# Optimization experiments

Hardware: AMD Instinct MI355X
Metric: run time of the kernel (lower is better)

The kernel has to match this reference:

```python
import jax, jax.numpy as jnp
import numpy as np

N_NODES = 50000
N_EDGES = 1600000
D_IN = 64
D_OUT = 64
N_REL = 32


def setup_inputs() -> dict:
    key = jax.random.key(0)
    k_h, k_w, k_src, k_dst, k_rel, k_norm = jax.random.split(key, 6)
    h = jax.random.normal(k_h, (N_NODES, D_IN), dtype=jnp.float32)
    W = jax.random.normal(k_w, (N_REL, D_IN, D_OUT), dtype=jnp.float32) * 0.05
    src = jax.random.randint(k_src, (N_EDGES,), 0, N_NODES, dtype=jnp.int32)
    dst = jax.random.randint(k_dst, (N_EDGES,), 0, N_NODES, dtype=jnp.int32)
    rel_type = jax.random.randint(k_rel, (N_EDGES,), 0, N_REL, dtype=jnp.int32)
    norm = jax.random.uniform(k_norm, (N_EDGES,), dtype=jnp.float32)
    return {"h": h, "W": W, "src": src, "dst": dst, "rel_type": rel_type, "norm": norm}


def reference(h, W, src, dst, rel_type, norm):
    # R-GCN message passing (is_input=False branch):
    #   msg_e = (W[rel_type_e] applied to h[src_e]) * norm_e
    #   h'_v  = sum_{e: dst_e = v} msg_e
    # Instead of gathering a [E, D_IN, D_OUT] weight tensor per edge (26 GB),
    # precompute h @ W for all (node, relation) pairs -- mathematically
    # identical since W[r] h[n] = (hW)[n, r] -- then gather per edge.
    n_nodes = h.shape[0]
    per_node_rel = jnp.einsum('ni,rio->nro', h, W)            # [N, R, D_OUT]
    msg = per_node_rel[src, rel_type] * norm[:, None]         # [E, D_OUT]
    out = jax.ops.segment_sum(msg, dst, num_segments=n_nodes)  # [N, D_OUT]
    return out
```

## Files before the change

### kernel.cpp

```cpp
#include <hip/hip_runtime.h>


#define N_NODES 50000
#define N_EDGES 1600000
#define D 64
#define N_REL 32

#define BSHIFT 7
#define NPB 128
#define NB 391
#define EPB 4096
#define SC_BLOCKS 391
#define SORT_CAP 6144
#define NKEY 256

typedef __attribute__((ext_vector_type(8))) __bf16 bf16x8;
typedef __attribute__((ext_vector_type(4))) __bf16 bf16x4;
typedef __attribute__((ext_vector_type(4))) float f32x4;
typedef __attribute__((ext_vector_type(4))) _Float16 f16x4;

static __device__ inline unsigned short f16_bits(_Float16 v) {
    union { _Float16 f; unsigned short u; } cv; cv.f = v; return cv.u;
}
static __device__ inline _Float16 bits_f16(unsigned short u) {
    union { _Float16 f; unsigned short u; } cv; cv.u = u; return cv.f;
}


__global__ __launch_bounds__(512) void k_zeroc(int* __restrict__ gcnt) {
    if (threadIdx.x < NB) gcnt[threadIdx.x] = 0;
}

__global__ __launch_bounds__(256) void k_hist2(const int* __restrict__ dst,
                                               int* __restrict__ gcnt) {
    __shared__ int lc[NB];
    for (int b = threadIdx.x; b < NB; b += 256) lc[b] = 0;
    __syncthreads();
    const int e0 = blockIdx.x * EPB;
    #pragma unroll
    for (int j = 0; j < 16; ++j) {
        int e = e0 + j * 256 + threadIdx.x;
        if (e < N_EDGES) atomicAdd(&lc[dst[e] >> BSHIFT], 1);
    }
    __syncthreads();
    for (int b = threadIdx.x; b < NB; b += 256)
        if (lc[b]) atomicAdd(&gcnt[b], lc[b]);
}

__global__ __launch_bounds__(512) void k_scanc(const int* __restrict__ gcnt,
                                               int* __restrict__ base,
                                               int* __restrict__ cur) {
    const int t = threadIdx.x;
    const int lane = t & 63;
    const int w = t >> 6;
    int v = (t < NB) ? gcnt[t] : 0;
    int x = v;
    #pragma unroll
    for (int d = 1; d < 64; d <<= 1) {
        int n = __shfl_up(x, d, 64);
        if (lane >= d) x += n;
    }
    __shared__ int wt[8];
    if (lane == 63) wt[w] = x;
    __syncthreads();
    if (t == 0) {
        int run = 0;
        #pragma unroll
        for (int i = 0; i < 8; ++i) { int tmp = wt[i]; wt[i] = run; run += tmp; }
    }
    __syncthreads();
    int excl = x - v + wt[w];
    if (t < NB) { base[t] = excl; cur[t] = excl; }
    if (t == NB - 1) base[NB] = excl + v;
}

__global__ __launch_bounds__(256) void k_scatter2(
        const int* __restrict__ src, const int* __restrict__ dst,
        const int* __restrict__ rel, const float* __restrict__ norm,
        int* __restrict__ cur, int2* __restrict__ pay) {
    __shared__ int cnt[NB];
    __shared__ int bl[NB + 1];
    __shared__ int gb[NB];
    __shared__ unsigned short bid[EPB];
    __shared__ int2 stage[EPB];
    __shared__ int wt[8];

    const int t = threadIdx.x;
    const int lane = t & 63;
    const int w = t >> 6;
    const int e0 = blockIdx.x * EPB;

    for (int b = t; b < NB; b += 256) cnt[b] = 0;
    __syncthreads();

    #pragma unroll
    for (int j = 0; j < 16; ++j) {
        int e = e0 + j * 256 + t;
        if (e < N_EDGES) atomicAdd(&cnt[dst[e] >> BSHIFT], 1);
    }
    __syncthreads();

    {
        int x0 = (t < NB) ? cnt[t] : 0;
        int x1 = (t + 256 < NB) ? cnt[t + 256] : 0;
        int s0 = x0, s1 = x1;
        #pragma unroll
        for (int d = 1; d < 64; d <<= 1) {
            int n0 = __shfl_up(s0, d, 64);
            int n1 = __shfl_up(s1, d, 64);
            if (lane >= d) { s0 += n0; s1 += n1; }
        }
        if (lane == 63) { wt[w] = s0; wt[4 + w] = s1; }
        __syncthreads();
        if (t == 0) {
            int run = 0;
            #pragma unroll
            for (int i = 0; i < 8; ++i) { int tmp = wt[i]; wt[i] = run; run += tmp; }
        }
        __syncthreads();
        int ex0 = s0 - x0 + wt[w];
        int ex1 = s1 - x1 + wt[4 + w];
        if (t < NB) bl[t] = ex0;
        if (t + 256 < NB) bl[t + 256] = ex1;
        if (t == 0) {
            int tot = (e0 + EPB <= N_EDGES) ? EPB : (N_EDGES > e0 ? N_EDGES - e0 : 0);
            bl[NB] = tot;
        }
    }
    __syncthreads();

    for (int b = t; b < NB; b += 256) {
        int c = bl[b + 1] - bl[b];
        gb[b] = c ? atomicAdd(&cur[b], c) : 0;
    }
    for (int b = t; b < NB; b += 256) cnt[b] = 0;
    __syncthreads();

    #pragma unroll
    for (int j = 0; j < 16; ++j) {
        int e = e0 + j * 256 + t;
        if (e < N_EDGES) {
            int dv = dst[e];
            int b = dv >> BSHIFT;
            int r = atomicAdd(&cnt[b], 1);
            int pos = bl[b] + r;
            stage[pos] = make_int2(((dv & (NPB - 1)) << 21) | (rel[e] << 16) | src[e],
                                   __float_as_int(norm[e]));
            bid[pos] = (unsigned short)b;
        }
    }
    __syncthreads();

    const int total = bl[NB];
    for (int p = t; p < total; p += 256) {
        int b = bid[p];
        pay[gb[b] + (p - bl[b])] = stage[p];
    }
}

__global__ __launch_bounds__(512) void k_sort(
        const int* __restrict__ base, int2* __restrict__ pay,
        int* __restrict__ runs) {
    __shared__ int2 stage[SORT_CAP];
    __shared__ int cnt[8][NKEY];
    __shared__ int wb[8][NKEY];
    __shared__ int kbase[NKEY];
    __shared__ int wsum[8];

    const int t = threadIdx.x;
    const int lane = t & 63;
    const int w = t >> 6;
    const int b = blockIdx.x;
    const int s = base[b];
    const int e = base[b + 1];
    const int n = min(e - s, SORT_CAP);

    for (int j = t; j < 8 * NKEY; j += 512) ((int*)cnt)[j] = 0;
    __syncthreads();

    for (int j = t; j < n; j += 512) {
        int2 p = pay[s + j];
        stage[j] = p;
        int key = (((p.x >> 25) & 7) << 5) | ((p.x >> 16) & 31);
        atomicAdd(&cnt[w][key], 1);
    }
    __syncthreads();

    int tot = 0;
    if (t < NKEY) {
        #pragma unroll
        for (int ww = 0; ww < 8; ++ww) tot += cnt[ww][t];
    }
    int x = tot;
    #pragma unroll
    for (int d = 1; d < 64; d <<= 1) {
        int nn = __shfl_up(x, d, 64);
        if (lane >= d) x += nn;
    }
    if (lane == 63) wsum[w] = x;
    __syncthreads();
    if (t == 0) {
        int run = 0;
        #pragma unroll
        for (int i = 0; i < 8; ++i) { int tmp = wsum[i]; wsum[i] = run; run += tmp; }
    }
    __syncthreads();
    int excl = x - tot + wsum[w];
    if (t < NKEY) kbase[t] = excl;
    __syncthreads();

    if (t < NKEY) {
        int run = kbase[t];
        #pragma unroll
        for (int ww = 0; ww < 8; ++ww) { wb[ww][t] = run; run += cnt[ww][t]; }
        runs[b * (NKEY + 1) + t] = s + kbase[t];
    }
    if (t == 0) runs[b * (NKEY + 1) + NKEY] = s + n;
    __syncthreads();
    for (int j = t; j < 8 * NKEY; j += 512) ((int*)cnt)[j] = 0;
    __syncthreads();

    for (int j = t; j < n; j += 512) {
        int2 p = stage[j];
        int key = (((p.x >> 25) & 7) << 5) | ((p.x >> 16) & 31);
        int pos = wb[w][key] + atomicAdd(&cnt[w][key], 1);
        pay[s + pos] = p;
    }
}

__global__ __launch_bounds__(256) void k_wconv(const float* __restrict__ W,
                                               __bf16* __restrict__ Wfrag) {
    const int r = blockIdx.x;
    const int lane = threadIdx.x & 63;
    const int jj = (threadIdx.x >> 6) * 2;
    const int q = lane >> 4;
    const int m = lane & 15;
    const float* Wr = W + (size_t)r * D * D;
    #pragma unroll
    for (int kt = 0; kt < 2; ++kt) {
        #pragma unroll
        for (int ot = 0; ot < 4; ++ot) {
            size_t dbase = ((((size_t)r * 2 + kt) * 4 + ot) * 64 + lane) * 8 + jj;
            Wfrag[dbase]     = (__bf16)Wr[(kt * 32 + q * 8 + jj) * D + ot * 16 + m];
            Wfrag[dbase + 1] = (__bf16)Wr[(kt * 32 + q * 8 + jj + 1) * D + ot * 16 + m];
        }
    }
}

__global__ __launch_bounds__(512) void k_hconv(const float* __restrict__ h,
                                               __bf16* __restrict__ hbf) {
    int idx = blockIdx.x * 512 + threadIdx.x;
    if (idx < N_NODES * 16) {
        float4 v = ((const float4*)h)[idx];
        bf16x4 o;
        o[0] = (__bf16)v.x; o[1] = (__bf16)v.y; o[2] = (__bf16)v.z; o[3] = (__bf16)v.w;
        ((bf16x4*)hbf)[idx] = o;
    }
}

__global__ __launch_bounds__(512) void k_fuse(
        const unsigned short* __restrict__ hbf, const __bf16* __restrict__ Wfrag,
        const int* __restrict__ runs, const int2* __restrict__ pay,
        float* __restrict__ out) {
    __shared__ int runsL[NKEY + 1];
    __shared__ __align__(16) unsigned short wbuf[2][4096];

    const int t = threadIdx.x;
    const int lane = t & 63;
    const int w = t >> 6;
    const int m = lane & 15;
    const int q = lane >> 4;
    const int b = blockIdx.x;

    for (int j = t; j < NKEY + 1; j += 512) runsL[j] = runs[b * (NKEY + 1) + j];
    ((bf16x8*)wbuf[0])[t] = ((const bf16x8*)Wfrag)[t];
    __syncthreads();

    const f32x4 vzero = {0.f, 0.f, 0.f, 0.f};
    f32x4 acc2[4];
    #pragma unroll
    for (int ot = 0; ot < 4; ++ot) acc2[ot] = vzero;

    const int kb = w * 32;

    int pr = 0, ptl = 0, prs = 0, pre_ = 0;
    while (pr < N_REL) { prs = runsL[kb + pr]; pre_ = runsL[kb + pr + 1]; if (pre_ > prs) break; ++pr; }

    int cr = N_REL, cmask = 0;
    int2 p_cur; bf16x8 a0c, a1c;
    int nrel = N_REL, nmask = 0;
    int2 p_nxt;

    if (pr < N_REL) {
        int ei = prs + ptl * 16 + m;
        p_cur = pay[min(ei, pre_ - 1)];
        cmask = (ei < pre_);
        cr = pr;
        ++ptl;
        if (prs + ptl * 16 >= pre_) {
            ++pr; ptl = 0;
            while (pr < N_REL) { prs = runsL[kb + pr]; pre_ = runsL[kb + pr + 1]; if (pre_ > prs) break; ++pr; }
        }
        const unsigned short* hrow = hbf + ((size_t)(p_cur.x & 0xFFFF) << 6);
        a0c = *(const bf16x8*)(hrow + q * 8);
        a1c = *(const bf16x8*)(hrow + 32 + q * 8);
        if (pr < N_REL) {
            int ei2 = prs + ptl * 16 + m;
            p_nxt = pay[min(ei2, pre_ - 1)];
            nmask = (ei2 < pre_);
            nrel = pr;
            ++ptl;
            if (prs + ptl * 16 >= pre_) {
                ++pr; ptl = 0;
                while (pr < N_REL) { prs = runsL[kb + pr]; pre_ = runsL[kb + pr + 1]; if (pre_ > prs) break; ++pr; }
            }
        }
    }

    for (int r = 0; r < N_REL; ++r) {
        bf16x8 stg;
        if (r + 1 < N_REL) stg = ((const bf16x8*)Wfrag)[(r + 1) * 512 + t];

        if (cr == r) {
            const unsigned short* wbp = wbuf[r & 1];
            bf16x8 wf[2][4];
            #pragma unroll
            for (int kt = 0; kt < 2; ++kt)
                #pragma unroll
                for (int ot = 0; ot < 4; ++ot)
                    wf[kt][ot] = *(const bf16x8*)(wbp + ((kt * 4 + ot) * 64 + lane) * 8);

            while (cr == r) {
                int2 p_b = p_nxt;
                int brel = nrel, bmask = nmask;
                bf16x8 a0n, a1n;
                if (brel < N_REL) {
                    const unsigned short* hrn = hbf + ((size_t)(p_b.x & 0xFFFF) << 6);
                    a0n = *(const bf16x8*)(hrn + q * 8);
                    a1n = *(const bf16x8*)(hrn + 32 + q * 8);
                }
                if (pr < N_REL) {
                    int ei2 = prs + ptl * 16 + m;
                    p_nxt = pay[min(ei2, pre_ - 1)];
                    nmask = (ei2 < pre_);
                    nrel = pr;
                    ++ptl;
                    if (prs + ptl * 16 >= pre_) {
                        ++pr; ptl = 0;
                        while (pr < N_REL) { prs = runsL[kb + pr]; pre_ = runsL[kb + pr + 1]; if (pre_ > prs) break; ++pr; }
                    }
                } else {
                    nrel = N_REL;
                }

                float nvf = cmask ? __int_as_float(p_cur.y) : 0.f;
                int meta = (((p_cur.x >> 21) & 15) << 16) | f16_bits((_Float16)nvf);

                f32x4 c1[4];
                #pragma unroll
                for (int ot = 0; ot < 4; ++ot) {
                    c1[ot] = __builtin_amdgcn_mfma_f32_16x16x32_bf16(a0c, wf[0][ot], vzero, 0, 0, 0);
                    c1[ot] = __builtin_amdgcn_mfma_f32_16x16x32_bf16(a1c, wf[1][ot], c1[ot], 0, 0, 0);
                }

                f16x4 a2;
                #pragma unroll
                for (int j = 0; j < 4; ++j) {
                    int sm = __shfl(meta, q * 4 + j, 64);
                    _Float16 nv = bits_f16((unsigned short)(sm & 0xFFFF));
                    a2[j] = ((sm >> 16) == m) ? nv : (_Float16)0.f;
                }

                #pragma unroll
                for (int ot = 0; ot < 4; ++ot) {
                    f16x4 b2;
                    b2[0] = (_Float16)c1[ot][0];
                    b2[1] = (_Float16)c1[ot][1];
                    b2[2] = (_Float16)c1[ot][2];
                    b2[3] = (_Float16)c1[ot][3];
                    acc2[ot] = __builtin_amdgcn_mfma_f32_16x16x16f16(a2, b2, acc2[ot], 0, 0, 0);
                }

                p_cur = p_b; cmask = bmask; cr = brel;
                a0c = a0n; a1c = a1n;
            }
        }

        if (r + 1 < N_REL) ((bf16x8*)wbuf[(r + 1) & 1])[t] = stg;
        __syncthreads();
    }

    const int node_base = b * NPB + w * 16;
    #pragma unroll
    for (int reg = 0; reg < 4; ++reg) {
        int node = node_base + q * 4 + reg;
        if (node < N_NODES) {
            float* orow = out + (size_t)node * D + m;
            #pragma unroll
            for (int ot = 0; ot < 4; ++ot)
                orow[ot * 16] = acc2[ot][reg];
        }
    }
}

extern "C" void kernel_launch(void* const* d_in, const int* in_sizes, int n_in,
                              void* d_out, int out_size, void* d_ws, size_t ws_size,
                              hipStream_t stream) {
    const float* h    = (const float*)d_in[0];
    const float* W    = (const float*)d_in[1];
    const int*   src  = (const int*)d_in[2];
    const int*   dst  = (const int*)d_in[3];
    const int*   rel  = (const int*)d_in[4];
    const float* norm = (const float*)d_in[5];
    float* out = (float*)d_out;

    char* ws = (char*)d_ws;
    int*    gcnt  = (int*)(ws);
    int*    base  = (int*)(ws + 0x1000);
    int*    cur   = (int*)(ws + 0x2000);
    int*    runs  = (int*)(ws + 0x3000);
    int2*   pay   = (int2*)(ws + 0x100000);
    __bf16* Wfrag = (__bf16*)(ws + 0xD40000);
    __bf16* hbf   = (__bf16*)(ws + 0xD80000);

    k_zeroc<<<1, 512, 0, stream>>>(gcnt);
    k_wconv<<<N_REL, 256, 0, stream>>>(W, Wfrag);
    k_hconv<<<1563, 512, 0, stream>>>(h, hbf);
    k_hist2<<<SC_BLOCKS, 256, 0, stream>>>(dst, gcnt);
    k_scanc<<<1, 512, 0, stream>>>(gcnt, base, cur);
    k_scatter2<<<SC_BLOCKS, 256, 0, stream>>>(src, dst, rel, norm, cur, pay);
    k_sort<<<NB, 512, 0, stream>>>(base, pay, runs);
    k_fuse<<<NB, 512, 0, stream>>>((const unsigned short*)hbf, Wfrag, runs, pay, out);
}
```

Before: 215.8 us.

## Replace histogram+scan with fixed-capacity buckets and fuse init kernels

Removes the destination histogram, scan and zeroing kernels by giving each bucket a fixed slot of capacity BCAP and initializing cursors to b*BCAP. Merges the h and W bf16 conversions and cursor init into a single launch. This cuts a full pass over dst, a serial scan kernel and several launch gaps, but assumes no bucket exceeds 6144 edges, and a skewed graph would overflow silently.

```diff
diff --git a/kernel.cpp b/kernel.cpp
--- a/kernel.cpp
+++ b/kernel.cpp
@@ -11,8 +11,12 @@
 #define NB 391
 #define EPB 4096
 #define SC_BLOCKS 391
+#define BCAP 6144
 #define SORT_CAP 6144
 #define NKEY 256
+
+#define HCONV_BLOCKS 1563
+#define INIT_BLOCKS (HCONV_BLOCKS + N_REL + 1)
 
 typedef __attribute__((ext_vector_type(8))) __bf16 bf16x8;
 typedef __attribute__((ext_vector_type(4))) __bf16 bf16x4;
@@ -27,51 +31,37 @@
 }
 
 
-__global__ __launch_bounds__(512) void k_zeroc(int* __restrict__ gcnt) {
-    if (threadIdx.x < NB) gcnt[threadIdx.x] = 0;
-}
-
-__global__ __launch_bounds__(256) void k_hist2(const int* __restrict__ dst,
-                                               int* __restrict__ gcnt) {
-    __shared__ int lc[NB];
-    for (int b = threadIdx.x; b < NB; b += 256) lc[b] = 0;
-    __syncthreads();
-    const int e0 = blockIdx.x * EPB;
-    #pragma unroll
-    for (int j = 0; j < 16; ++j) {
-        int e = e0 + j * 256 + threadIdx.x;
-        if (e < N_EDGES) atomicAdd(&lc[dst[e] >> BSHIFT], 1);
-    }
-    __syncthreads();
-    for (int b = threadIdx.x; b < NB; b += 256)
-        if (lc[b]) atomicAdd(&gcnt[b], lc[b]);
-}
-
-__global__ __launch_bounds__(512) void k_scanc(const int* __restrict__ gcnt,
-                                               int* __restrict__ base,
-                                               int* __restrict__ cur) {
-    const int t = threadIdx.x;
-    const int lane = t & 63;
-    const int w = t >> 6;
-    int v = (t < NB) ? gcnt[t] : 0;
-    int x = v;
-    #pragma unroll
-    for (int d = 1; d < 64; d <<= 1) {
-        int n = __shfl_up(x, d, 64);
-        if (lane >= d) x += n;
-    }
-    __shared__ int wt[8];
-    if (lane == 63) wt[w] = x;
-    __syncthreads();
-    if (t == 0) {
-        int run = 0;
-        #pragma unroll
-        for (int i = 0; i < 8; ++i) { int tmp = wt[i]; wt[i] = run; run += tmp; }
-    }
-    __syncthreads();
-    int excl = x - v + wt[w];
-    if (t < NB) { base[t] = excl; cur[t] = excl; }
-    if (t == NB - 1) base[NB] = excl + v;
+__global__ __launch_bounds__(512) void k_init(
+        const float* __restrict__ h, __bf16* __restrict__ hbf,
+        const float* __restrict__ W, __bf16* __restrict__ Wfrag,
+        int* __restrict__ cur) {
+    const int blk = blockIdx.x;
+    if (blk < HCONV_BLOCKS) {
+        int idx = blk * 512 + threadIdx.x;
+        if (idx < N_NODES * 16) {
+            float4 v = ((const float4*)h)[idx];
+            bf16x4 o;
+            o[0] = (__bf16)v.x; o[1] = (__bf16)v.y; o[2] = (__bf16)v.z; o[3] = (__bf16)v.w;
+            ((bf16x4*)hbf)[idx] = o;
+        }
+    } else if (blk < HCONV_BLOCKS + N_REL) {
+        const int r = blk - HCONV_BLOCKS;
+        const int lane = threadIdx.x & 63;
+        const int jj = threadIdx.x >> 6;
+        const int q = lane >> 4;
+        const int m = lane & 15;
+        const float* Wr = W + (size_t)r * D * D;
+        #pragma unroll
+        for (int kt = 0; kt < 2; ++kt) {
+            #pragma unroll
+            for (int ot = 0; ot < 4; ++ot) {
+                size_t dbase = ((((size_t)r * 2 + kt) * 4 + ot) * 64 + lane) * 8 + jj;
+                Wfrag[dbase] = (__bf16)Wr[(kt * 32 + q * 8 + jj) * D + ot * 16 + m];
+            }
+        }
+    } else {
+        if (threadIdx.x < NB) cur[threadIdx.x] = threadIdx.x * BCAP;
+    }
 }
 
 __global__ __launch_bounds__(256) void k_scatter2(
@@ -159,7 +149,7 @@
 }
 
 __global__ __launch_bounds__(512) void k_sort(
-        const int* __restrict__ base, int2* __restrict__ pay,
+        const int* __restrict__ cur, int2* __restrict__ pay,
         int* __restrict__ runs) {
     __shared__ int2 stage[SORT_CAP];
     __shared__ int cnt[8][NKEY];
@@ -171,8 +161,8 @@
     const int lane = t & 63;
     const int w = t >> 6;
     const int b = blockIdx.x;
-    const int s = base[b];
-    const int e = base[b + 1];
+    const int s = b * BCAP;
+    const int e = cur[b];
     const int n = min(e - s, SORT_CAP);
 
     for (int j = t; j < 8 * NKEY; j += 512) ((int*)cnt)[j] = 0;
@@ -225,36 +215,6 @@
         int key = (((p.x >> 25) & 7) << 5) | ((p.x >> 16) & 31);
         int pos = wb[w][key] + atomicAdd(&cnt[w][key], 1);
         pay[s + pos] = p;
-    }
-}
-
-__global__ __launch_bounds__(256) void k_wconv(const float* __restrict__ W,
-                                               __bf16* __restrict__ Wfrag) {
-    const int r = blockIdx.x;
-    const int lane = threadIdx.x & 63;
-    const int jj = (threadIdx.x >> 6) * 2;
-    const int q = lane >> 4;
-    const int m = lane & 15;
-    const float* Wr = W + (size_t)r * D * D;
-    #pragma unroll
-    for (int kt = 0; kt < 2; ++kt) {
-        #pragma unroll
-        for (int ot = 0; ot < 4; ++ot) {
-            size_t dbase = ((((size_t)r * 2 + kt) * 4 + ot) * 64 + lane) * 8 + jj;
-            Wfrag[dbase]     = (__bf16)Wr[(kt * 32 + q * 8 + jj) * D + ot * 16 + m];
-            Wfrag[dbase + 1] = (__bf16)Wr[(kt * 32 + q * 8 + jj + 1) * D + ot * 16 + m];
-        }
-    }
-}
-
-__global__ __launch_bounds__(512) void k_hconv(const float* __restrict__ h,
-                                               __bf16* __restrict__ hbf) {
-    int idx = blockIdx.x * 512 + threadIdx.x;
-    if (idx < N_NODES * 16) {
-        float4 v = ((const float4*)h)[idx];
-        bf16x4 o;
-        o[0] = (__bf16)v.x; o[1] = (__bf16)v.y; o[2] = (__bf16)v.z; o[3] = (__bf16)v.w;
-        ((bf16x4*)hbf)[idx] = o;
     }
 }
 
@@ -415,20 +375,14 @@
     float* out = (float*)d_out;
 
     char* ws = (char*)d_ws;
-    int*    gcnt  = (int*)(ws);
-    int*    base  = (int*)(ws + 0x1000);
     int*    cur   = (int*)(ws + 0x2000);
     int*    runs  = (int*)(ws + 0x3000);
     int2*   pay   = (int2*)(ws + 0x100000);
-    __bf16* Wfrag = (__bf16*)(ws + 0xD40000);
-    __bf16* hbf   = (__bf16*)(ws + 0xD80000);
-
-    k_zeroc<<<1, 512, 0, stream>>>(gcnt);
-    k_wconv<<<N_REL, 256, 0, stream>>>(W, Wfrag);
-    k_hconv<<<1563, 512, 0, stream>>>(h, hbf);
-    k_hist2<<<SC_BLOCKS, 256, 0, stream>>>(dst, gcnt);
-    k_scanc<<<1, 512, 0, stream>>>(gcnt, base, cur);
+    __bf16* Wfrag = (__bf16*)(ws + 0x1400000);
+    __bf16* hbf   = (__bf16*)(ws + 0x1480000);
+
+    k_init<<<INIT_BLOCKS, 512, 0, stream>>>(h, hbf, W, Wfrag, cur);
     k_scatter2<<<SC_BLOCKS, 256, 0, stream>>>(src, dst, rel, norm, cur, pay);
-    k_sort<<<NB, 512, 0, stream>>>(base, pay, runs);
+    k_sort<<<NB, 512, 0, stream>>>(cur, pay, runs);
     k_fuse<<<NB, 512, 0, stream>>>((const unsigned short*)hbf, Wfrag, runs, pay, out);
 }
```

Result: faster. 193.2 us (-10.5%).
